# Optimization experiments

Hardware: AMD Instinct MI355X
Metric: run time of the kernel (lower is better)

## Reference

```python
import math
import jax, jax.numpy as jnp
import numpy as np

V, D, H, L, F, S, B = 32000, 768, 12, 6, 3072, 2048, 4
DK = D // H


def setup_inputs() -> dict:
    key = jax.random.key(0)
    ks = jax.random.split(key, 16)
    sc = 0.02
    n = jax.random.normal
    inp = {
        "input_ids": jax.random.randint(ks[0], (B, S), 0, V, dtype=jnp.int64)
        if jax.config.jax_enable_x64 else jax.random.randint(ks[0], (B, S), 0, V, dtype=jnp.int32),
        "emb": n(ks[1], (V, D), jnp.float32) * sc,
        "Wq": n(ks[2], (L, D, D), jnp.float32) * sc, "bq": jnp.zeros((L, D), jnp.float32),
        "Wk": n(ks[3], (L, D, D), jnp.float32) * sc, "bk": jnp.zeros((L, D), jnp.float32),
        "Wv": n(ks[4], (L, D, D), jnp.float32) * sc, "bv": jnp.zeros((L, D), jnp.float32),
        "Wo": n(ks[5], (L, D, D), jnp.float32) * sc, "bo": jnp.zeros((L, D), jnp.float32),
        "W1": n(ks[6], (L, D, F), jnp.float32) * sc, "b1": jnp.zeros((L, F), jnp.float32),
        "W2": n(ks[7], (L, F, D), jnp.float32) * sc, "b2": jnp.zeros((L, D), jnp.float32),
        "gamma": jnp.ones((L, D), jnp.float32), "beta": jnp.zeros((L, D), jnp.float32),
    }
    return inp


def _pos_encoding(seq_len, d):
    pos = jnp.arange(seq_len, dtype=jnp.float32)[:, None]                  # [S,1]
    div = jnp.exp(jnp.arange(0, d, 2, dtype=jnp.float32) * (-math.log(10000.0) / d))
    ang = pos * div                                                        # [S,D/2]
    return jnp.stack([jnp.sin(ang), jnp.cos(ang)], axis=-1).reshape(seq_len, d)


def _layernorm(x, g, b, eps=1e-5):
    mu = x.mean(-1, keepdims=True)
    var = ((x - mu) ** 2).mean(-1, keepdims=True)
    return (x - mu) * jax.lax.rsqrt(var + eps) * g + b


def _forward(input_ids, emb, Wq, bq, Wk, bk, Wv, bv, Wo, bo, W1, b1, W2, b2, gamma, beta):
    mask = (input_ids != 1)[:, None, None, :]                              # [B,1,1,S]
    x = emb[input_ids] + _pos_encoding(input_ids.shape[1], emb.shape[1])   # [B,S,D]

    def layer(x, p):
        wq, bq_, wk, bk_, wv, bv_, wo, bo_, w1, b1_, w2, b2_, g, bt = p
        def heads(h):  # [B,S,D] -> [B,H,S,DK]
            return h.reshape(B, S, H, DK).transpose(0, 2, 1, 3)
        q = heads(x @ wq + bq_)
        k = heads(x @ wk + bk_)
        v = heads(x @ wv + bv_)
        scores = jnp.einsum("bhqd,bhkd->bhqk", q, k) / math.sqrt(DK)
        scores = jnp.where(mask, scores, -1e9)
        attn = jax.nn.softmax(scores, axis=-1)
        o = jnp.einsum("bhqk,bhkd->bhqd", attn, v)
        o = o.transpose(0, 2, 1, 3).reshape(B, S, D) @ wo + bo_
        x1 = _layernorm(x + o, g, bt)
        ff = jax.nn.relu(x1 @ w1 + b1_) @ w2 + b2_
        return _layernorm(x1 + ff, g, bt), None  # same norm params reused (as in source)

    x, _ = jax.lax.scan(layer, x, (Wq, bq, Wk, bk, Wv, bv, Wo, bo, W1, b1, W2, b2, gamma, beta))
    return x.mean(axis=1)                                                  # [B,D]


def reference(input_ids, emb, Wq, bq, Wk, bk, Wv, bv, Wo, bo, W1, b1, W2, b2, gamma, beta):
    return _forward(input_ids, emb, Wq, bq, Wk, bk, Wv, bv, Wo, bo, W1, b1, W2, b2, gamma, beta)
```

## Files before the change

### kernel.cpp

```cpp
#include <hip/hip_runtime.h>
#include <hip/hip_bf16.h>
#include <math.h>

typedef unsigned short u16;
typedef unsigned long long u64;
using bf16x8 = __attribute__((ext_vector_type(8))) short;
using f32x4  = __attribute__((ext_vector_type(4))) float;

static constexpr int kD = 768;
static constexpr int kH = 12;
static constexpr int kL = 6;
static constexpr int kF = 3072;
static constexpr int kS = 2048;
static constexpr int kB = 4;
static constexpr int kQW = 2304;
static constexpr int kNT = kB * kS;

static constexpr float kQScale = 0.18033688011112043f;

__device__ __forceinline__ u16 f2bf(float f) {
    return __bfloat16_as_ushort(__float2bfloat16(f));
}
__device__ __forceinline__ float b2f(u16 u) {
    return __uint_as_float((unsigned)u << 16);
}
__device__ __forceinline__ unsigned cvtpk(float a, float b) {
    unsigned d;
    asm volatile("v_cvt_pk_bf16_f32 %0, %1, %2" : "=v"(d) : "v"(a), "v"(b));
    return d;
}
__device__ __forceinline__ float exp2fast(float x) {
#if __has_builtin(__builtin_amdgcn_exp2f)
    return __builtin_amdgcn_exp2f(x);
#else
    return __expf(x * 0.6931471805599453f);
#endif
}

__device__ __forceinline__ void gload16(const void* g, void* l) {
    auto gp = reinterpret_cast<const __attribute__((address_space(1))) unsigned int*>(
        reinterpret_cast<uintptr_t>(g));
    auto lp = reinterpret_cast<__attribute__((address_space(3))) unsigned int*>(
        reinterpret_cast<uintptr_t>(l));
    __builtin_amdgcn_global_load_lds(gp, lp, 16, 0, 0);
}

__global__ __launch_bounds__(256) void embed_pe(
    const int* __restrict__ ids, const float* __restrict__ emb,
    u16* __restrict__ xbf)
{
    const int t = blockIdx.x;
    const int s = t & (kS - 1);
    const int id = ids[t];
#pragma unroll
    for (int j = 0; j < 3; ++j) {
        const int d = threadIdx.x + (j << 8);
        const float i2 = (float)((d >> 1) << 1);
        const float dv = __expf(i2 * (-9.210340371976184f / 768.f));
        const float ang = (float)s * dv;
        const float pe = (d & 1) ? cosf(ang) : sinf(ang);
        xbf[(size_t)t * kD + d] = f2bf(emb[(size_t)id * kD + d] + pe);
    }
}

__global__ __launch_bounds__(256) void embed_pe_f32(
    const int* __restrict__ ids, const float* __restrict__ emb,
    float* __restrict__ x)
{
    const int t = blockIdx.x;
    const int s = t & (kS - 1);
    const int id = ids[t];
#pragma unroll
    for (int j = 0; j < 3; ++j) {
        const int d = threadIdx.x + (j << 8);
        const float i2 = (float)((d >> 1) << 1);
        const float dv = __expf(i2 * (-9.210340371976184f / 768.f));
        const float ang = (float)s * dv;
        const float pe = (d & 1) ? cosf(ang) : sinf(ang);
        x[(size_t)t * kD + d] = emb[(size_t)id * kD + d] + pe;
    }
}

__global__ __launch_bounds__(64) void mk_maskbits(const int* __restrict__ ids,
                                                  u64* __restrict__ mbits)
{
    const int w = blockIdx.x;
    const int lane = threadIdx.x;
    const u64 m = __ballot(ids[(size_t)w * 64 + lane] != 1);
    if (lane == 0) mbits[w] = m;
}

__global__ __launch_bounds__(256) void bias_build(
    const float* __restrict__ bq, const float* __restrict__ bk,
    const float* __restrict__ bv, const float* __restrict__ bo,
    const float* __restrict__ b1, const float* __restrict__ b2,
    float* __restrict__ ba)
{
    const int i = blockIdx.x * 256 + threadIdx.x;
    if (i >= 6 * 6912) return;
    const int l = i / 6912, p = i % 6912;
    float v;
    if      (p < 768)  v = bq[l * 768 + p] * kQScale;
    else if (p < 1536) v = bk[l * 768 + p - 768];
    else if (p < 2304) v = bv[l * 768 + p - 1536];
    else if (p < 3072) v = bo[l * 768 + p - 2304];
    else if (p < 6144) v = b1[(size_t)l * 3072 + p - 3072];
    else               v = b2[l * 768 + p - 6144];
    ba[i] = v;
}

static constexpr size_t OFF_WO = (size_t)2304 * 768;
static constexpr size_t OFF_W1 = OFF_WO + (size_t)768 * 768;
static constexpr size_t OFF_W2 = OFF_W1 + (size_t)3072 * 768;
static constexpr size_t WARENA_E = OFF_W2 + (size_t)768 * 3072;

__global__ __launch_bounds__(256) void cvt_all(
    const float* __restrict__ Wq, const float* __restrict__ Wk,
    const float* __restrict__ Wv, const float* __restrict__ Wo,
    const float* __restrict__ W1, const float* __restrict__ W2,
    u16* __restrict__ wa)
{
    __shared__ float T[64][68];
    const int t = blockIdx.x;
    const float* S; u16* Dp; int Nsrc, Kdst, srow0, scol0; float sc = 1.f;
    if (t < 432) {
        const int ni = t % 36, ki = t / 36;
        const int ng = ni * 64;
        const int sel = ng / 768;
        scol0 = ng % 768; srow0 = ki * 64;
        S = (sel == 0) ? Wq : (sel == 1) ? Wk : Wv;
        if (sel == 0) sc = kQScale;
        Nsrc = 768; Kdst = 768;
        Dp = wa + (size_t)ng * 768 + srow0;
    } else if (t < 576) {
        const int tt = t - 432; const int ni = tt % 12, ki = tt / 12;
        scol0 = ni * 64; srow0 = ki * 64;
        S = Wo; Nsrc = 768; Kdst = 768;
        Dp = wa + OFF_WO + (size_t)(ni * 64) * 768 + srow0;
    } else if (t < 1152) {
        const int tt = t - 576; const int ni = tt % 48, ki = tt / 48;
        scol0 = ni * 64; srow0 = ki * 64;
        S = W1; Nsrc = 3072; Kdst = 768;
        Dp = wa + OFF_W1 + (size_t)(ni * 64) * 768 + srow0;
    } else {
        const int tt = t - 1152; const int ni = tt % 12, ki = tt / 12;
        scol0 = ni * 64; srow0 = ki * 64;
        S = W2; Nsrc = 768; Kdst = 3072;
        Dp = wa + OFF_W2 + (size_t)(ni * 64) * 3072 + srow0;
    }
    const int tid = threadIdx.x;
#pragma unroll
    for (int i = 0; i < 4; ++i) {
        const int idx = tid + (i << 8);
        const int kr = idx >> 4;
        const int nc = (idx & 15) << 2;
        const float4 v = *(const float4*)(S + (size_t)(srow0 + kr) * Nsrc + scol0 + nc);
        T[kr][nc] = v.x; T[kr][nc + 1] = v.y; T[kr][nc + 2] = v.z; T[kr][nc + 3] = v.w;
    }
    __syncthreads();
#pragma unroll
    for (int i = 0; i < 4; ++i) {
        const int idx = tid + (i << 8);
        const int nr = idx >> 4;
        const int kc = (idx & 15) << 2;
        ushort4 o;
        o.x = f2bf(T[kc][nr] * sc);     o.y = f2bf(T[kc + 1][nr] * sc);
        o.z = f2bf(T[kc + 2][nr] * sc); o.w = f2bf(T[kc + 3][nr] * sc);
        *(ushort4*)(Dp + (size_t)nr * Kdst + kc) = o;
    }
}

__global__ __launch_bounds__(256, 2) void gemm256b(
    const u16* __restrict__ A, const u16* __restrict__ Bt,
    const float* __restrict__ bias, void* __restrict__ Cv,
    u16* __restrict__ vTp, int M, int N, int K, int mode)
{
    __shared__ u16 As[2][4096];
    __shared__ u16 Bs[2][8192];
    const int tid = threadIdx.x;
    const int l = tid & 63;
    const int lo = l & 15, hi = l >> 4;
    const int wc = tid >> 6;

    int brow = blockIdx.x, bcol = blockIdx.y;
    const int gx = gridDim.x;
    if ((gx & 7) == 0) {
        const int id = blockIdx.y * gx + blockIdx.x;
        const int xcd = id & 7, idx = id >> 3;
        const int rpx = gx >> 3;
        brow = xcd * rpx + (idx % rpx);
        bcol = idx / rpx;
    }
    const size_t row0 = (size_t)brow * 128;
    const size_t col0 = (size_t)bcol * 256;

    const int ca0 = tid, ca1 = tid + 256;
    const int ra0 = ca0 >> 2, ga0 = (ca0 & 3) ^ ((ra0 >> 1) & 3);
    const int ra1 = ca1 >> 2, ga1 = (ca1 & 3) ^ ((ra1 >> 1) & 3);
    const u16* aP0 = A + (row0 + ra0) * K + ga0 * 8;
    const u16* aP1 = A + (row0 + ra1) * K + ga1 * 8;
    const u16* bP[4];
#pragma unroll
    for (int q = 0; q < 4; ++q) {
        const int c = tid + (q << 8);
        const int r = c >> 2, g = (c & 3) ^ ((r >> 1) & 3);
        bP[q] = Bt + (col0 + r) * K + g * 8;
    }

    f32x4 acc[8][4];
#pragma unroll
    for (int i = 0; i < 8; ++i)
#pragma unroll
        for (int j = 0; j < 4; ++j)
#pragma unroll
            for (int r = 0; r < 4; ++r) acc[i][j][r] = 0.f;

    int aoff[8], boff[4];
#pragma unroll
    for (int i = 0; i < 8; ++i) {
        const int ra = i * 16 + lo;
        aoff[i] = ra * 32 + ((hi ^ ((ra >> 1) & 3)) << 3);
    }
#pragma unroll
    for (int j = 0; j < 4; ++j) {
        const int rb = wc * 64 + j * 16 + lo;
        boff[j] = rb * 32 + ((hi ^ ((rb >> 1) & 3)) << 3);
    }

    const int NT = K >> 5;
    gload16(aP0, As[0] + ca0 * 8);
    gload16(aP1, As[0] + ca1 * 8);
#pragma unroll
    for (int q = 0; q < 4; ++q) gload16(bP[q], Bs[0] + (tid + (q << 8)) * 8);

    for (int t = 0; t < NT; ++t) {
        const int cur = t & 1;
        if (t + 1 < NT) {
            const int k0 = (t + 1) << 5;
            const int nb = cur ^ 1;
            gload16(aP0 + k0, As[nb] + ca0 * 8);
            gload16(aP1 + k0, As[nb] + ca1 * 8);
#pragma unroll
            for (int q = 0; q < 4; ++q)
                gload16(bP[q] + k0, Bs[nb] + (tid + (q << 8)) * 8);
            asm volatile("s_waitcnt vmcnt(6)" ::: "memory");
        } else {
            asm volatile("s_waitcnt vmcnt(0)" ::: "memory");
        }
        __builtin_amdgcn_s_barrier();
        bf16x8 af[8], bfr[4];
#pragma unroll
        for (int i = 0; i < 8; ++i) af[i]  = *(const bf16x8*)&As[cur][aoff[i]];
#pragma unroll
        for (int j = 0; j < 4; ++j) bfr[j] = *(const bf16x8*)&Bs[cur][boff[j]];
        __builtin_amdgcn_s_setprio(1);
#pragma unroll
        for (int i = 0; i < 8; ++i)
#pragma unroll
            for (int j = 0; j < 4; ++j)
                acc[i][j] = __builtin_amdgcn_mfma_f32_16x16x32_bf16(
                    af[i], bfr[j], acc[i][j], 0, 0, 0);
        __builtin_amdgcn_s_setprio(0);
        asm volatile("s_waitcnt lgkmcnt(0)" ::: "memory");
        __builtin_amdgcn_sched_barrier(0);
        __builtin_amdgcn_s_barrier();
    }

    const bool vmode = (mode == 3) && (col0 >= 1536);
    if (vmode) {
#pragma unroll
        for (int i = 0; i < 8; ++i) {
            const size_t rbase = row0 + i * 16 + hi * 4;
            const size_t tb = (rbase >> 6) * 64;
            const int k0 = (int)(rbase & 63);
            const int pos = (((k0 >> 2) & 3) << 3) + (((k0 >> 4) & 1) << 2)
                          + ((k0 >> 5) << 5);
#pragma unroll
            for (int j = 0; j < 4; ++j) {
                const size_t c = col0 + wc * 64 + j * 16 + lo;
                const float bs = bias[c];
                const size_t d = c - 1536;
                ushort4 o;
                o.x = f2bf(acc[i][j][0] + bs);
                o.y = f2bf(acc[i][j][1] + bs);
                o.z = f2bf(acc[i][j][2] + bs);
                o.w = f2bf(acc[i][j][3] + bs);
                *(ushort4*)(vTp + d * (size_t)M + tb + pos) = o;
            }
        }
        return;
    }

#pragma unroll
    for (int i = 0; i < 8; ++i) {
        const size_t rbase = row0 + i * 16 + hi * 4;
#pragma unroll
        for (int j = 0; j < 4; ++j) {
            const size_t c = col0 + wc * 64 + j * 16 + lo;
            const float bs = bias[c];
#pragma unroll
            for (int r = 0; r < 4; ++r) {
                float v = acc[i][j][r] + bs;
                if (mode == 2) v = fmaxf(v, 0.f);
                ((u16*)Cv)[(rbase + r) * (size_t)N + c] = f2bf(v);
            }
        }
    }
}

__global__ __launch_bounds__(256) void gemm_bf16(
    const u16* __restrict__ A, const u16* __restrict__ Bt,
    const float* __restrict__ bias, void* __restrict__ Cv,
    u16* __restrict__ vTp, int M, int N, int K, int mode)
{
    __shared__ u16 As[2][4096];
    __shared__ u16 Bs[2][4096];
    const int tid = threadIdx.x;
    const int l = tid & 63;
    const int lo = l & 15, hi = l >> 4;
    const int w = tid >> 6, wr = w >> 1, wc = w & 1;

    int brow = blockIdx.x, bcol = blockIdx.y;
    const int gx = gridDim.x;
    if ((gx & 7) == 0) {
        const int id = blockIdx.y * gx + blockIdx.x;
        const int xcd = id & 7, idx = id >> 3;
        const int rpx = gx >> 3;
        brow = xcd * rpx + (idx % rpx);
        bcol = idx / rpx;
    }
    const size_t row0 = (size_t)brow * 128;
    const size_t col0 = (size_t)bcol * 128;

    const int c0 = tid, c1 = tid + 256;
    const int r0 = c0 >> 2, g0 = (c0 & 3) ^ ((r0 >> 1) & 3);
    const int r1 = c1 >> 2, g1 = (c1 & 3) ^ ((r1 >> 1) & 3);
    const u16* a0 = A  + (row0 + r0) * K + g0 * 8;
    const u16* a1 = A  + (row0 + r1) * K + g1 * 8;
    const u16* b0 = Bt + (col0 + r0) * K + g0 * 8;
    const u16* b1 = Bt + (col0 + r1) * K + g1 * 8;

    f32x4 acc[4][4];
#pragma unroll
    for (int i = 0; i < 4; ++i)
#pragma unroll
        for (int j = 0; j < 4; ++j)
#pragma unroll
            for (int r = 0; r < 4; ++r) acc[i][j][r] = 0.f;

    int aoff[4], boff[4];
#pragma unroll
    for (int i = 0; i < 4; ++i) {
        const int ra = wr * 64 + i * 16 + lo;
        aoff[i] = ra * 32 + ((hi ^ ((ra >> 1) & 3)) << 3);
        const int rb = wc * 64 + i * 16 + lo;
        boff[i] = rb * 32 + ((hi ^ ((rb >> 1) & 3)) << 3);
    }

    const int NT = K >> 5;
    gload16(a0, As[0] + c0 * 8);
    gload16(a1, As[0] + c1 * 8);
    gload16(b0, Bs[0] + c0 * 8);
    gload16(b1, Bs[0] + c1 * 8);

    int cur = 0;
    for (int t = 0; t < NT; ++t) {
        if (t + 1 < NT) {
            const int k0 = (t + 1) << 5;
            const int nb = cur ^ 1;
            gload16(a0 + k0, As[nb] + c0 * 8);
            gload16(a1 + k0, As[nb] + c1 * 8);
            gload16(b0 + k0, Bs[nb] + c0 * 8);
            gload16(b1 + k0, Bs[nb] + c1 * 8);
            asm volatile("s_waitcnt vmcnt(4)" ::: "memory");
        } else {
            asm volatile("s_waitcnt vmcnt(0)" ::: "memory");
        }
        __builtin_amdgcn_s_barrier();
        bf16x8 af[4], bfr[4];
#pragma unroll
        for (int i = 0; i < 4; ++i) af[i]  = *(const bf16x8*)&As[cur][aoff[i]];
#pragma unroll
        for (int j = 0; j < 4; ++j) bfr[j] = *(const bf16x8*)&Bs[cur][boff[j]];
#pragma unroll
        for (int i = 0; i < 4; ++i)
#pragma unroll
            for (int j = 0; j < 4; ++j)
                acc[i][j] = __builtin_amdgcn_mfma_f32_16x16x32_bf16(
                    af[i], bfr[j], acc[i][j], 0, 0, 0);
        asm volatile("s_waitcnt lgkmcnt(0)" ::: "memory");
        __builtin_amdgcn_sched_barrier(0);
        __builtin_amdgcn_s_barrier();
        cur ^= 1;
    }

#pragma unroll
    for (int i = 0; i < 4; ++i) {
        const size_t rbase = row0 + wr * 64 + i * 16 + hi * 4;
#pragma unroll
        for (int j = 0; j < 4; ++j) {
            const size_t c = col0 + wc * 64 + j * 16 + lo;
            const float bs = bias[c];
#pragma unroll
            for (int r = 0; r < 4; ++r) {
                float v = acc[i][j][r] + bs;
                if (mode == 2) v = fmaxf(v, 0.f);
                ((u16*)Cv)[(rbase + r) * (size_t)N + c] = f2bf(v);
            }
        }
    }
}

__global__ __launch_bounds__(512) void attn_mfma(
    const u16* __restrict__ QKV, const u16* __restrict__ vT,
    const u64* __restrict__ mbits, u16* __restrict__ O)
{
    __shared__ u16 Ks[2][4096];
    __shared__ u16 Vs[2][4096];

    const int tid = threadIdx.x, l = tid & 63, w = tid >> 6;
    const int lo = l & 15, hi = l >> 4;

    const int flat = blockIdx.x + 16 * (blockIdx.y + 12 * blockIdx.z);
    const int nf = (flat & 7) * 96 + (flat >> 3);
    const int qi = nf & 15;
    const int h  = (nf >> 4) % 12;
    const int b  = nf / 192;
    const int q0 = qi << 7;

    bf16x8 qf0, qf1;
    {
        const u16* qp = QKV + ((size_t)(b * kS + q0 + w * 16 + lo)) * kQW
                            + h * 64 + hi * 8;
        qf0 = *(const bf16x8*)qp;
        qf1 = *(const bf16x8*)(qp + 32);
    }

    const int rw = tid >> 3, sx = tid & 7, E = sx ^ (rw & 7);
    const u16* Kbase = QKV + (size_t)(b * kS) * kQW + 768 + h * 64;
    const u16* Vbase = vT + (size_t)(h * 64) * kNT + b * kS;

    f32x4 accO[4];
#pragma unroll
    for (int n = 0; n < 4; ++n)
#pragma unroll
        for (int r = 0; r < 4; ++r) accO[n][r] = 0.f;
    float m = -3.0e38f, lsum = 0.f;

    const int ksw = (lo & 7) << 3;
    constexpr int NTt = kS / 64;

    gload16(Kbase + (size_t)rw * kQW + E * 8, Ks[0] + tid * 8);
    gload16(Vbase + (size_t)rw * kNT + E * 8, Vs[0] + tid * 8);

    int cur = 0;
    for (int kt = 0; kt < NTt; ++kt) {
        asm volatile("s_waitcnt vmcnt(0)" ::: "memory");
        __syncthreads();

        if (kt + 1 < NTt) {
            const size_t kof = (size_t)((kt + 1) << 6) * kQW;
            const size_t vof = (size_t)((kt + 1) << 6);
            gload16(Kbase + kof + (size_t)rw * kQW + E * 8, Ks[cur ^ 1] + tid * 8);
            gload16(Vbase + (size_t)rw * kNT + vof + E * 8, Vs[cur ^ 1] + tid * 8);
        }

        f32x4 st[4];
        __builtin_amdgcn_s_setprio(1);
#pragma unroll
        for (int j = 0; j < 4; ++j) {
#pragma unroll
            for (int r = 0; r < 4; ++r) st[j][r] = 0.f;
            const int kb2 = (j * 16 + lo) * 64;
            const bf16x8 k0 = *(const bf16x8*)&Ks[cur][kb2 + ((hi * 8)      ^ ksw)];
            const bf16x8 k1 = *(const bf16x8*)&Ks[cur][kb2 + ((hi * 8 + 32) ^ ksw)];
            st[j] = __builtin_amdgcn_mfma_f32_16x16x32_bf16(k0, qf0, st[j], 0, 0, 0);
            st[j] = __builtin_amdgcn_mfma_f32_16x16x32_bf16(k1, qf1, st[j], 0, 0, 0);
        }
        __builtin_amdgcn_s_setprio(0);

        float rmax = st[0][0];
#pragma unroll
        for (int j = 0; j < 4; ++j)
#pragma unroll
            for (int r = 0; r < 4; ++r) rmax = fmaxf(rmax, st[j][r]);
        rmax = fmaxf(rmax, __shfl_xor(rmax, 16));
        rmax = fmaxf(rmax, __shfl_xor(rmax, 32));

        const bool skip = __all(rmax <= m + 11.0f);
        if (!skip) {
            const float mn = fmaxf(m, rmax);
            const float corr = exp2fast(m - mn);
            m = mn;
            lsum *= corr;
            float c2[4];
#pragma unroll
            for (int r = 0; r < 4; ++r) c2[r] = __shfl(corr, hi * 4 + r);
#pragma unroll
            for (int n = 0; n < 4; ++n)
#pragma unroll
                for (int r = 0; r < 4; ++r) accO[n][r] *= c2[r];
        }

#pragma unroll
        for (int j = 0; j < 4; ++j)
#pragma unroll
            for (int r = 0; r < 4; ++r) st[j][r] = exp2fast(st[j][r] - m);

        const u64 mb = mbits[b * 32 + kt];
        if (mb != ~0ull) {
#pragma unroll
            for (int j = 0; j < 4; ++j)
#pragma unroll
                for (int r = 0; r < 4; ++r)
                    if (!((mb >> (j * 16 + hi * 4 + r)) & 1)) st[j][r] = 0.f;
        }

        float ts = 0.f;
#pragma unroll
        for (int j = 0; j < 4; ++j)
#pragma unroll
            for (int r = 0; r < 4; ++r) ts += st[j][r];
        ts += __shfl_xor(ts, 16);
        ts += __shfl_xor(ts, 32);
        lsum += ts;

        union PU { unsigned u[4]; bf16x8 v; } p0, p1;
        p0.u[0] = cvtpk(st[0][0], st[0][1]); p0.u[1] = cvtpk(st[0][2], st[0][3]);
        p0.u[2] = cvtpk(st[1][0], st[1][1]); p0.u[3] = cvtpk(st[1][2], st[1][3]);
        p1.u[0] = cvtpk(st[2][0], st[2][1]); p1.u[1] = cvtpk(st[2][2], st[2][3]);
        p1.u[2] = cvtpk(st[3][0], st[3][1]); p1.u[3] = cvtpk(st[3][2], st[3][3]);

        __builtin_amdgcn_s_setprio(1);
#pragma unroll
        for (int n = 0; n < 4; ++n) {
            const int vb2 = (n * 16 + lo) * 64;
            const bf16x8 v0 = *(const bf16x8*)&Vs[cur][vb2 + ((hi * 8)      ^ ksw)];
            const bf16x8 v1 = *(const bf16x8*)&Vs[cur][vb2 + ((hi * 8 + 32) ^ ksw)];
            accO[n] = __builtin_amdgcn_mfma_f32_16x16x32_bf16(p0.v, v0, accO[n], 0, 0, 0);
            accO[n] = __builtin_amdgcn_mfma_f32_16x16x32_bf16(p1.v, v1, accO[n], 0, 0, 0);
        }
        __builtin_amdgcn_s_setprio(0);
        cur ^= 1;
    }

    float linv[4];
#pragma unroll
    for (int r = 0; r < 4; ++r) linv[r] = 1.f / __shfl(lsum, hi * 4 + r);
#pragma unroll
    for (int n = 0; n < 4; ++n)
#pragma unroll
        for (int r = 0; r < 4; ++r)
            O[((size_t)(b * kS + q0 + w * 16 + hi * 4 + r)) * kD
              + h * 64 + n * 16 + lo] = f2bf(accO[n][r] * linv[r]);
}

__global__ __launch_bounds__(256) void add_ln_bf(
    const u16* __restrict__ a, const u16* __restrict__ r,
    const float* __restrict__ g, const float* __restrict__ bt,
    u16* __restrict__ out)
{
    const int lane = threadIdx.x & 63;
    const size_t row = (size_t)blockIdx.x * 4 + (threadIdx.x >> 6);
    const ushort4* a4 = (const ushort4*)(a + row * kD);
    const ushort4* r4 = (const ushort4*)(r + row * kD);
    float v[3][4];
    float s = 0.f;
#pragma unroll
    for (int j = 0; j < 3; ++j) {
        const ushort4 av = a4[j * 64 + lane];
        const ushort4 rv = r4[j * 64 + lane];
        v[j][0] = b2f(av.x) + b2f(rv.x);
        v[j][1] = b2f(av.y) + b2f(rv.y);
        v[j][2] = b2f(av.z) + b2f(rv.z);
        v[j][3] = b2f(av.w) + b2f(rv.w);
        s += v[j][0] + v[j][1] + v[j][2] + v[j][3];
    }
#pragma unroll
    for (int off = 32; off; off >>= 1) s += __shfl_xor(s, off);
    const float mu = s * (1.f / 768.f);
    float vs = 0.f;
#pragma unroll
    for (int j = 0; j < 3; ++j)
#pragma unroll
        for (int e = 0; e < 4; ++e) {
            const float t0 = v[j][e] - mu;
            vs = fmaf(t0, t0, vs);
        }
#pragma unroll
    for (int off = 32; off; off >>= 1) vs += __shfl_xor(vs, off);
    const float rstd = rsqrtf(vs * (1.f / 768.f) + 1e-5f);
    const float4* g4 = (const float4*)g;
    const float4* b4 = (const float4*)bt;
#pragma unroll
    for (int j = 0; j < 3; ++j) {
        const float4 gv = g4[j * 64 + lane];
        const float4 bv = b4[j * 64 + lane];
        ushort4 o;
        o.x = f2bf((v[j][0] - mu) * rstd * gv.x + bv.x);
        o.y = f2bf((v[j][1] - mu) * rstd * gv.y + bv.y);
        o.z = f2bf((v[j][2] - mu) * rstd * gv.z + bv.z);
        o.w = f2bf((v[j][3] - mu) * rstd * gv.w + bv.w);
        ((ushort4*)(out + row * kD))[j * 64 + lane] = o;
    }
}

__global__ __launch_bounds__(192) void mean_part_bf(
    const u16* __restrict__ x, float* __restrict__ mred)
{
    const int c = blockIdx.x, b = blockIdx.y;
    const int d = threadIdx.x * 4;
    const u16* base = x + ((size_t)b * kS + c * 32) * kD + d;
    float s0 = 0.f, s1 = 0.f, s2 = 0.f, s3 = 0.f;
#pragma unroll 8
    for (int t = 0; t < 32; ++t) {
        const ushort4 u = *(const ushort4*)(base + (size_t)t * kD);
        s0 += b2f(u.x); s1 += b2f(u.y); s2 += b2f(u.z); s3 += b2f(u.w);
    }
    float4 o; o.x = s0; o.y = s1; o.z = s2; o.w = s3;
    *(float4*)(mred + ((size_t)b * 64 + c) * kD + d) = o;
}

__global__ __launch_bounds__(256) void mean_fin(
    const float* __restrict__ mred, float* __restrict__ out)
{
    const int d = blockIdx.x * 256 + threadIdx.x;
    const int b = blockIdx.y;
    float s = 0.f;
#pragma unroll
    for (int c = 0; c < 64; ++c) s += mred[((size_t)b * 64 + c) * kD + d];
    out[b * kD + d] = s * (1.f / 2048.f);
}

__global__ __launch_bounds__(256) void add_ln_f32(
    const float* __restrict__ a, const float* __restrict__ r,
    const float* __restrict__ g, const float* __restrict__ bt,
    float* __restrict__ out)
{
    const int lane = threadIdx.x & 63;
    const size_t row = (size_t)blockIdx.x * 4 + (threadIdx.x >> 6);
    const float4* a4 = (const float4*)(a + row * kD);
    const float4* r4 = (const float4*)(r + row * kD);
    float4 v[3];
    float s = 0.f;
#pragma unroll
    for (int j = 0; j < 3; ++j) {
        const float4 av = a4[j * 64 + lane];
        const float4 rv = r4[j * 64 + lane];
        v[j].x = av.x + rv.x; v[j].y = av.y + rv.y;
        v[j].z = av.z + rv.z; v[j].w = av.w + rv.w;
        s += v[j].x + v[j].y + v[j].z + v[j].w;
    }
#pragma unroll
    for (int off = 32; off; off >>= 1) s += __shfl_xor(s, off);
    const float mu = s * (1.f / 768.f);
    float vs = 0.f;
#pragma unroll
    for (int j = 0; j < 3; ++j) {
        float t0 = v[j].x - mu, t1 = v[j].y - mu, t2 = v[j].z - mu, t3 = v[j].w - mu;
        vs = fmaf(t0, t0, fmaf(t1, t1, fmaf(t2, t2, fmaf(t3, t3, vs))));
    }
#pragma unroll
    for (int off = 32; off; off >>= 1) vs += __shfl_xor(vs, off);
    const float rstd = rsqrtf(vs * (1.f / 768.f) + 1e-5f);
    const float4* g4 = (const float4*)g;
    const float4* b4 = (const float4*)bt;
#pragma unroll
    for (int j = 0; j < 3; ++j) {
        const float4 gv = g4[j * 64 + lane];
        const float4 bv = b4[j * 64 + lane];
        float4 o;
        o.x = (v[j].x - mu) * rstd * gv.x + bv.x;
        o.y = (v[j].y - mu) * rstd * gv.y + bv.y;
        o.z = (v[j].z - mu) * rstd * gv.z + bv.z;
        o.w = (v[j].w - mu) * rstd * gv.w + bv.w;
        ((float4*)(out + row * kD))[j * 64 + lane] = o;
    }
}

__global__ __launch_bounds__(256) void mean_s(
    const float* __restrict__ x, float* __restrict__ out)
{
    const int d = blockIdx.x * 256 + threadIdx.x;
    const int b = blockIdx.y;
    float s = 0.f;
    for (int t = 0; t < kS; ++t) s += x[((size_t)b * kS + t) * kD + d];
    out[b * kD + d] = s * (1.f / 2048.f);
}

__global__ __launch_bounds__(256) void gemm_f32(
    const float* __restrict__ A, const float* __restrict__ W,
    const float* __restrict__ bias, float* __restrict__ C,
    int M, int N, int K, int relu)
{
    __shared__ float As[16][68];
    __shared__ float Bs[16][68];
    const int tid = threadIdx.x;
    const int row0 = blockIdx.x << 6;
    const int col0 = blockIdx.y << 6;
    const int tx = tid & 15, ty = tid >> 4;
    const int ar = tid >> 2;
    const int ak = (tid & 3) << 2;
    const int bk = tid >> 4;
    const int bc = (tid & 15) << 2;
    float acc[4][4] = {};
    const float* Ap = A + (size_t)(row0 + ar) * K + ak;
    const float* Wp = W + (size_t)bk * N + col0 + bc;
    for (int k0 = 0; k0 < K; k0 += 16) {
        const float4 a4 = *(const float4*)(Ap + k0);
        const float4 b4 = *(const float4*)(Wp + (size_t)k0 * N);
        __syncthreads();
        As[ak + 0][ar] = a4.x; As[ak + 1][ar] = a4.y;
        As[ak + 2][ar] = a4.z; As[ak + 3][ar] = a4.w;
        *(float4*)&Bs[bk][bc] = b4;
        __syncthreads();
#pragma unroll
        for (int kk = 0; kk < 16; ++kk) {
            const float4 av = *(const float4*)&As[kk][ty << 2];
            const float4 bv = *(const float4*)&Bs[kk][tx << 2];
            const float aa[4] = {av.x, av.y, av.z, av.w};
            const float bb[4] = {bv.x, bv.y, bv.z, bv.w};
#pragma unroll
            for (int i = 0; i < 4; ++i)
#pragma unroll
                for (int j = 0; j < 4; ++j)
                    acc[i][j] = fmaf(aa[i], bb[j], acc[i][j]);
        }
    }
#pragma unroll
    for (int i = 0; i < 4; ++i) {
        const int row = row0 + (ty << 2) + i;
#pragma unroll
        for (int j = 0; j < 4; ++j) {
            const int col = col0 + (tx << 2) + j;
            float v = acc[i][j] + bias[col];
            if (relu) v = fmaxf(v, 0.f);
            C[(size_t)row * N + col] = v;
        }
    }
}

__global__ __launch_bounds__(256) void attn_fused(
    const float* __restrict__ Q, const float* __restrict__ Km,
    const float* __restrict__ Vm, const int* __restrict__ ids,
    float* __restrict__ O)
{
    __shared__ float Ksf[64 * 64];
    __shared__ float Vtf[64 * 64];
    __shared__ float Qs[16][64];
    __shared__ float Psf[4][4][64];
    const int tid = threadIdx.x;
    const int w = tid >> 6;
    const int lane = tid & 63;
    const int h = blockIdx.y, b = blockIdx.z;
    const int qrow0 = blockIdx.x << 4;
    {
        const int r = tid >> 4;
        const int c4 = tid & 15;
        const float4 q4 = *(const float4*)(
            Q + ((size_t)(b * kS + qrow0 + r)) * kD + h * 64 + (c4 << 2));
        Qs[r][(c4 << 2) + 0] = q4.x * 0.125f;
        Qs[r][(c4 << 2) + 1] = q4.y * 0.125f;
        Qs[r][(c4 << 2) + 2] = q4.z * 0.125f;
        Qs[r][(c4 << 2) + 3] = q4.w * 0.125f;
    }
    float m[4], lsum[4], o[4];
#pragma unroll
    for (int r = 0; r < 4; ++r) { m[r] = -3.0e38f; lsum[r] = 0.f; o[r] = 0.f; }
    for (int kt = 0; kt < kS / 64; ++kt) {
        __syncthreads();
#pragma unroll
        for (int i = 0; i < 4; ++i) {
            const int lin = tid + (i << 8);
            const int row = lin >> 4;
            const int s4 = lin & 15;
            const size_t gro = ((size_t)(b * kS + (kt << 6) + row)) * kD + h * 64 + (s4 << 2);
            const float4 k4 = *(const float4*)(Km + gro);
            ((float4*)Ksf)[(row << 4) + (s4 ^ (row & 7))] = k4;
            const float4 v4 = *(const float4*)(Vm + gro);
            const int ksl = row >> 2, ke = row & 3;
            const int d0 = s4 << 2;
            Vtf[(d0 + 0) * 64 + ((ksl ^ ((d0 + 0) & 7)) << 2) + ke] = v4.x;
            Vtf[(d0 + 1) * 64 + ((ksl ^ ((d0 + 1) & 7)) << 2) + ke] = v4.y;
            Vtf[(d0 + 2) * 64 + ((ksl ^ ((d0 + 2) & 7)) << 2) + ke] = v4.z;
            Vtf[(d0 + 3) * 64 + ((ksl ^ ((d0 + 3) & 7)) << 2) + ke] = v4.w;
        }
        __syncthreads();
        const bool masked = (ids[(size_t)b * kS + (kt << 6) + lane] == 1);
        float scr[4] = {0.f, 0.f, 0.f, 0.f};
#pragma unroll
        for (int i16 = 0; i16 < 16; ++i16) {
            const float4 kv = ((const float4*)Ksf)[(lane << 4) + (i16 ^ (lane & 7))];
#pragma unroll
            for (int r = 0; r < 4; ++r) {
                const float4 qv = *(const float4*)&Qs[(w << 2) + r][i16 << 2];
                scr[r] = fmaf(kv.x, qv.x, fmaf(kv.y, qv.y,
                          fmaf(kv.z, qv.z, fmaf(kv.w, qv.w, scr[r]))));
            }
        }
#pragma unroll
        for (int r = 0; r < 4; ++r) {
            float sm = masked ? -3.0e38f : scr[r];
#pragma unroll
            for (int off = 32; off; off >>= 1) sm = fmaxf(sm, __shfl_xor(sm, off));
            const float mn = fmaxf(m[r], sm);
            const float cr = __expf(m[r] - mn);
            const float pv = masked ? 0.f : __expf(scr[r] - mn);
            float ps = pv;
#pragma unroll
            for (int off = 32; off; off >>= 1) ps += __shfl_xor(ps, off);
            lsum[r] = lsum[r] * cr + ps;
            o[r] *= cr;
            m[r] = mn;
            Psf[w][r][lane] = pv;
        }
#pragma unroll
        for (int i16 = 0; i16 < 16; ++i16) {
            const float4 vv = ((const float4*)Vtf)[(lane << 4) + (i16 ^ (lane & 7))];
#pragma unroll
            for (int r = 0; r < 4; ++r) {
                const float4 pv = *(const float4*)&Psf[w][r][i16 << 2];
                o[r] = fmaf(pv.x, vv.x, fmaf(pv.y, vv.y,
                        fmaf(pv.z, vv.z, fmaf(pv.w, vv.w, o[r]))));
            }
        }
    }
#pragma unroll
    for (int r = 0; r < 4; ++r)
        O[((size_t)(b * kS + qrow0 + (w << 2) + r)) * kD + h * 64 + lane] =
            o[r] / lsum[r];
}

extern "C" void kernel_launch(void* const* d_in, const int* in_sizes, int n_in,
                              void* d_out, int out_size, void* d_ws, size_t ws_size,
                              hipStream_t stream)
{
    const int*   ids   = (const int*)  d_in[0];
    const float* emb   = (const float*)d_in[1];
    const float* Wq    = (const float*)d_in[2];
    const float* bq    = (const float*)d_in[3];
    const float* Wk    = (const float*)d_in[4];
    const float* bk    = (const float*)d_in[5];
    const float* Wv    = (const float*)d_in[6];
    const float* bv    = (const float*)d_in[7];
    const float* Wo    = (const float*)d_in[8];
    const float* bo    = (const float*)d_in[9];
    const float* W1    = (const float*)d_in[10];
    const float* b1    = (const float*)d_in[11];
    const float* W2    = (const float*)d_in[12];
    const float* b2    = (const float*)d_in[13];
    const float* gamma = (const float*)d_in[14];
    const float* beta  = (const float*)d_in[15];
    float* out = (float*)d_out;

    const size_t BUFE = (size_t)kB * kS * kD;
    const size_t WDD  = (size_t)kD * kD;
    const size_t WDF  = (size_t)kD * kF;
    const size_t HIDE = (size_t)kB * kS * kF;
    const int NTOK = kB * kS;

    const size_t NEED = BUFE * 2 * 4
                      + HIDE * 2
                      + WARENA_E * 2
                      + (size_t)6 * 6912 * 4
                      + 128 * 8
                      + (size_t)kB * 64 * kD * 4;

    if (ws_size >= NEED) {
        u16*   xb  = (u16*)d_ws;
        u16*   x1b = xb + BUFE;
        u16*   ao  = x1b + BUFE;
        u16*   ob  = ao + BUFE;
        u16*   sc  = ob + BUFE;
        u16*   vtb = sc + (size_t)NTOK * kQW;
        u16*   wa  = sc + HIDE;
        float* ba  = (float*)(wa + WARENA_E);
        u64*   mbt = (u64*)(ba + 6 * 6912);
        float* mrd = (float*)(mbt + 128);

        embed_pe<<<NTOK, 256, 0, stream>>>(ids, emb, xb);
        mk_maskbits<<<kB * kS / 64, 64, 0, stream>>>(ids, mbt);
        bias_build<<<(6 * 6912 + 255) / 256, 256, 0, stream>>>(
            bq, bk, bv, bo, b1, b2, ba);

        for (int l = 0; l < kL; ++l) {
            const size_t oDD = (size_t)l * WDD;
            const size_t oDF = (size_t)l * WDF;
            const float* bl = ba + (size_t)l * 6912;
            const float* gl  = gamma + (size_t)l * kD;
            const float* btl = beta  + (size_t)l * kD;

            cvt_all<<<1728, 256, 0, stream>>>(
                Wq + oDD, Wk + oDD, Wv + oDD, Wo + oDD, W1 + oDF, W2 + oDF, wa);

            gemm256b<<<dim3(64, 9), 256, 0, stream>>>(
                xb, wa, bl, sc, vtb, NTOK, kQW, kD, 3);

            attn_mfma<<<dim3(kS / 128, kH, kB), 512, 0, stream>>>(
                sc, vtb, mbt, ao);

            gemm_bf16<<<dim3(64, 6), 256, 0, stream>>>(
                ao, wa + OFF_WO, bl + 2304, ob, nullptr, NTOK, kD, kD, 1);

            add_ln_bf<<<NTOK / 4, 256, 0, stream>>>(xb, ob, gl, btl, x1b);

            gemm256b<<<dim3(64, 12), 256, 0, stream>>>(
                x1b, wa + OFF_W1, bl + 3072, sc, nullptr, NTOK, kF, kD, 2);
            gemm_bf16<<<dim3(64, 6), 256, 0, stream>>>(
                sc, wa + OFF_W2, bl + 6144, ob, nullptr, NTOK, kD, kF, 1);

            add_ln_bf<<<NTOK / 4, 256, 0, stream>>>(x1b, ob, gl, btl, xb);
        }

        mean_part_bf<<<dim3(64, kB), 192, 0, stream>>>(xb, mrd);
        mean_fin<<<dim3(kD / 256, kB), 256, 0, stream>>>(mrd, out);
        return;
    }

    if (ws_size < 5 * BUFE * sizeof(float)) return;
    float* xb = (float*)d_ws;
    float* kb = xb + BUFE;
    float* qb = kb + BUFE;
    float* vb = qb + BUFE;
    float* obf = vb + BUFE;
    float* hb = qb;

    embed_pe_f32<<<NTOK, 256, 0, stream>>>(ids, emb, xb);
    for (int l = 0; l < kL; ++l) {
        const size_t oDD = (size_t)l * WDD;
        const size_t oDF = (size_t)l * WDF;
        gemm_f32<<<dim3(NTOK / 64, kD / 64), 256, 0, stream>>>(
            xb, Wq + oDD, bq + (size_t)l * kD, qb, NTOK, kD, kD, 0);
        gemm_f32<<<dim3(NTOK / 64, kD / 64), 256, 0, stream>>>(
            xb, Wk + oDD, bk + (size_t)l * kD, kb, NTOK, kD, kD, 0);
        gemm_f32<<<dim3(NTOK / 64, kD / 64), 256, 0, stream>>>(
            xb, Wv + oDD, bv + (size_t)l * kD, vb, NTOK, kD, kD, 0);
        attn_fused<<<dim3(kS / 16, kH, kB), 256, 0, stream>>>(qb, kb, vb, ids, obf);
        gemm_f32<<<dim3(NTOK / 64, kD / 64), 256, 0, stream>>>(
            obf, Wo + oDD, bo + (size_t)l * kD, qb, NTOK, kD, kD, 0);
        add_ln_f32<<<NTOK / 4, 256, 0, stream>>>(xb, qb,
            gamma + (size_t)l * kD, beta + (size_t)l * kD, kb);
        for (int c = 0; c < 2; ++c) {
            const size_t ro = (size_t)c * 4096;
            gemm_f32<<<dim3(4096 / 64, kF / 64), 256, 0, stream>>>(
                kb + ro * kD, W1 + oDF, b1 + (size_t)l * kF, hb, 4096, kF, kD, 1);
            gemm_f32<<<dim3(4096 / 64, kD / 64), 256, 0, stream>>>(
                hb, W2 + oDF, b2 + (size_t)l * kD, obf + ro * kD, 4096, kD, kF, 0);
        }
        add_ln_f32<<<NTOK / 4, 256, 0, stream>>>(kb, obf,
            gamma + (size_t)l * kD, beta + (size_t)l * kD, xb);
    }
    mean_s<<<dim3(kD / 256, kB), 256, 0, stream>>>(xb, out);
}
```

Measured before the change: 1.521 ms.

## Triple-buffer LDS tiles in GEMM and attention kernels, drop second barrier

Converts the double-buffered shared-memory pipelines in both GEMM kernels and the attention kernel into three-stage ring buffers. Loads are issued two tiles ahead, and the per-iteration trailing LDS wait and second barrier are removed, since the buffer being refilled was last read an iteration earlier. This deepens global-load latency hiding and cuts synchronisation per K-step. It also raises shared memory per block by half, which could lower occupancy, especially for the 256-wide GEMM tile. It adds a priority hint around the MFMA block in the smaller GEMM.

```diff
diff --git a/kernel.cpp b/kernel.cpp
--- a/kernel.cpp
+++ b/kernel.cpp
@@ -175,8 +175,8 @@
     const float* __restrict__ bias, void* __restrict__ Cv,
     u16* __restrict__ vTp, int M, int N, int K, int mode)
 {
-    __shared__ u16 As[2][4096];
-    __shared__ u16 Bs[2][8192];
+    __shared__ u16 As[3][4096];
+    __shared__ u16 Bs[3][8192];
     const int tid = threadIdx.x;
     const int l = tid & 63;
     const int lo = l & 15, hi = l >> 4;
@@ -228,26 +228,33 @@
     }
 
     const int NT = K >> 5;
-    gload16(aP0, As[0] + ca0 * 8);
-    gload16(aP1, As[0] + ca1 * 8);
-#pragma unroll
-    for (int q = 0; q < 4; ++q) gload16(bP[q], Bs[0] + (tid + (q << 8)) * 8);
-
+#pragma unroll
+    for (int t = 0; t < 2; ++t) {
+        const int k0 = t << 5;
+        gload16(aP0 + k0, As[t] + ca0 * 8);
+        gload16(aP1 + k0, As[t] + ca1 * 8);
+#pragma unroll
+        for (int q = 0; q < 4; ++q)
+            gload16(bP[q] + k0, Bs[t] + (tid + (q << 8)) * 8);
+    }
+
+    int cur = 0;
     for (int t = 0; t < NT; ++t) {
-        const int cur = t & 1;
         if (t + 1 < NT) {
-            const int k0 = (t + 1) << 5;
-            const int nb = cur ^ 1;
-            gload16(aP0 + k0, As[nb] + ca0 * 8);
-            gload16(aP1 + k0, As[nb] + ca1 * 8);
-#pragma unroll
-            for (int q = 0; q < 4; ++q)
-                gload16(bP[q] + k0, Bs[nb] + (tid + (q << 8)) * 8);
             asm volatile("s_waitcnt vmcnt(6)" ::: "memory");
         } else {
             asm volatile("s_waitcnt vmcnt(0)" ::: "memory");
         }
         __builtin_amdgcn_s_barrier();
+        if (t + 2 < NT) {
+            const int k0 = (t + 2) << 5;
+            const int nb = (cur + 2 >= 3) ? cur - 1 : cur + 2;
+            gload16(aP0 + k0, As[nb] + ca0 * 8);
+            gload16(aP1 + k0, As[nb] + ca1 * 8);
+#pragma unroll
+            for (int q = 0; q < 4; ++q)
+                gload16(bP[q] + k0, Bs[nb] + (tid + (q << 8)) * 8);
+        }
         bf16x8 af[8], bfr[4];
 #pragma unroll
         for (int i = 0; i < 8; ++i) af[i]  = *(const bf16x8*)&As[cur][aoff[i]];
@@ -261,9 +268,7 @@
                 acc[i][j] = __builtin_amdgcn_mfma_f32_16x16x32_bf16(
                     af[i], bfr[j], acc[i][j], 0, 0, 0);
         __builtin_amdgcn_s_setprio(0);
-        asm volatile("s_waitcnt lgkmcnt(0)" ::: "memory");
-        __builtin_amdgcn_sched_barrier(0);
-        __builtin_amdgcn_s_barrier();
+        cur = (cur + 1 == 3) ? 0 : cur + 1;
     }
 
     const bool vmode = (mode == 3) && (col0 >= 1536);
@@ -313,8 +318,8 @@
     const float* __restrict__ bias, void* __restrict__ Cv,
     u16* __restrict__ vTp, int M, int N, int K, int mode)
 {
-    __shared__ u16 As[2][4096];
-    __shared__ u16 Bs[2][4096];
+    __shared__ u16 As[3][4096];
+    __shared__ u16 Bs[3][4096];
     const int tid = threadIdx.x;
     const int l = tid & 63;
     const int lo = l & 15, hi = l >> 4;
@@ -358,40 +363,45 @@
     }
 
     const int NT = K >> 5;
-    gload16(a0, As[0] + c0 * 8);
-    gload16(a1, As[0] + c1 * 8);
-    gload16(b0, Bs[0] + c0 * 8);
-    gload16(b1, Bs[0] + c1 * 8);
+#pragma unroll
+    for (int t = 0; t < 2; ++t) {
+        const int k0 = t << 5;
+        gload16(a0 + k0, As[t] + c0 * 8);
+        gload16(a1 + k0, As[t] + c1 * 8);
+        gload16(b0 + k0, Bs[t] + c0 * 8);
+        gload16(b1 + k0, Bs[t] + c1 * 8);
+    }
 
     int cur = 0;
     for (int t = 0; t < NT; ++t) {
         if (t + 1 < NT) {
-            const int k0 = (t + 1) << 5;
-            const int nb = cur ^ 1;
+            asm volatile("s_waitcnt vmcnt(4)" ::: "memory");
+        } else {
+            asm volatile("s_waitcnt vmcnt(0)" ::: "memory");
+        }
+        __builtin_amdgcn_s_barrier();
+        if (t + 2 < NT) {
+            const int k0 = (t + 2) << 5;
+            const int nb = (cur + 2 >= 3) ? cur - 1 : cur + 2;
             gload16(a0 + k0, As[nb] + c0 * 8);
             gload16(a1 + k0, As[nb] + c1 * 8);
             gload16(b0 + k0, Bs[nb] + c0 * 8);
             gload16(b1 + k0, Bs[nb] + c1 * 8);
-            asm volatile("s_waitcnt vmcnt(4)" ::: "memory");
-        } else {
-            asm volatile("s_waitcnt vmcnt(0)" ::: "memory");
-        }
-        __builtin_amdgcn_s_barrier();
+        }
         bf16x8 af[4], bfr[4];
 #pragma unroll
         for (int i = 0; i < 4; ++i) af[i]  = *(const bf16x8*)&As[cur][aoff[i]];
 #pragma unroll
         for (int j = 0; j < 4; ++j) bfr[j] = *(const bf16x8*)&Bs[cur][boff[j]];
+        __builtin_amdgcn_s_setprio(1);
 #pragma unroll
         for (int i = 0; i < 4; ++i)
 #pragma unroll
             for (int j = 0; j < 4; ++j)
                 acc[i][j] = __builtin_amdgcn_mfma_f32_16x16x32_bf16(
                     af[i], bfr[j], acc[i][j], 0, 0, 0);
-        asm volatile("s_waitcnt lgkmcnt(0)" ::: "memory");
-        __builtin_amdgcn_sched_barrier(0);
-        __builtin_amdgcn_s_barrier();
-        cur ^= 1;
+        __builtin_amdgcn_s_setprio(0);
+        cur = (cur + 1 == 3) ? 0 : cur + 1;
     }
 
 #pragma unroll
@@ -415,8 +425,8 @@
     const u16* __restrict__ QKV, const u16* __restrict__ vT,
     const u64* __restrict__ mbits, u16* __restrict__ O)
 {
-    __shared__ u16 Ks[2][4096];
-    __shared__ u16 Vs[2][4096];
+    __shared__ u16 Ks[3][4096];
+    __shared__ u16 Vs[3][4096];
 
     const int tid = threadIdx.x, l = tid & 63, w = tid >> 6;
     const int lo = l & 15, hi = l >> 4;
@@ -450,19 +460,29 @@
     const int ksw = (lo & 7) << 3;
     constexpr int NTt = kS / 64;
 
-    gload16(Kbase + (size_t)rw * kQW + E * 8, Ks[0] + tid * 8);
-    gload16(Vbase + (size_t)rw * kNT + E * 8, Vs[0] + tid * 8);
+#pragma unroll
+    for (int t = 0; t < 2; ++t) {
+        const size_t kof = (size_t)(t << 6) * kQW;
+        const size_t vof = (size_t)(t << 6);
+        gload16(Kbase + kof + (size_t)rw * kQW + E * 8, Ks[t] + tid * 8);
+        gload16(Vbase + (size_t)rw * kNT + vof + E * 8, Vs[t] + tid * 8);
+    }
 
     int cur = 0;
     for (int kt = 0; kt < NTt; ++kt) {
-        asm volatile("s_waitcnt vmcnt(0)" ::: "memory");
+        if (kt + 1 < NTt) {
+            asm volatile("s_waitcnt vmcnt(2)" ::: "memory");
+        } else {
+            asm volatile("s_waitcnt vmcnt(0)" ::: "memory");
+        }
         __syncthreads();
 
-        if (kt + 1 < NTt) {
-            const size_t kof = (size_t)((kt + 1) << 6) * kQW;
-            const size_t vof = (size_t)((kt + 1) << 6);
-            gload16(Kbase + kof + (size_t)rw * kQW + E * 8, Ks[cur ^ 1] + tid * 8);
-            gload16(Vbase + (size_t)rw * kNT + vof + E * 8, Vs[cur ^ 1] + tid * 8);
+        if (kt + 2 < NTt) {
+            const size_t kof = (size_t)((kt + 2) << 6) * kQW;
+            const size_t vof = (size_t)((kt + 2) << 6);
+            const int nb = (cur + 2 >= 3) ? cur - 1 : cur + 2;
+            gload16(Kbase + kof + (size_t)rw * kQW + E * 8, Ks[nb] + tid * 8);
+            gload16(Vbase + (size_t)rw * kNT + vof + E * 8, Vs[nb] + tid * 8);
         }
 
         f32x4 st[4];
@@ -541,7 +561,7 @@
             accO[n] = __builtin_amdgcn_mfma_f32_16x16x32_bf16(p1.v, v1, accO[n], 0, 0, 0);
         }
         __builtin_amdgcn_s_setprio(0);
-        cur ^= 1;
+        cur = (cur + 1 == 3) ? 0 : cur + 1;
     }
 
     float linv[4];
```

Measured after the change: 1.528 ms. No clear change (+0.5%).
